# Kernel optimization log

Measured on AMD Instinct MI355X. Metric: run time of the kernel, lower is better.

Reference implementation:

```python
import jax, jax.numpy as jnp
import numpy as np

B, S, D = 32, 8192, 64


def setup_inputs() -> dict:
    key = jax.random.key(0)
    k1, k2 = jax.random.split(key)
    input_real = jax.random.normal(k1, (B, S, D), dtype=jnp.float32)
    input_imag = jax.random.normal(k2, (B, S, D), dtype=jnp.float32)
    return {"input_real": input_real, "input_imag": input_imag}


def reference(input_real, input_imag):
    # ComplexMixture: mean over seq of per-token complex outer products v v^H.
    # Original builds [B,S,D,D] via 4 batch_dots then means over S; fused here
    # as Gram contractions over the sequence axis (no [B,S,D,D] intermediate).
    seq_len = input_real.shape[1]
    inv_s = jnp.asarray(1.0 / seq_len, dtype=input_real.dtype)
    rr = jnp.einsum('bsi,bsj->bij', input_real, input_real)
    ii = jnp.einsum('bsi,bsj->bij', input_imag, input_imag)
    ri = jnp.einsum('bsi,bsj->bij', input_real, input_imag)
    out_real = (rr + ii) * inv_s                     # [B, D, D], symmetric
    out_imag = (ri - jnp.swapaxes(ri, 1, 2)) * inv_s  # [B, D, D], antisymmetric
    return (out_real, out_imag)
```

## Files before the change

kernel.cpp:

```cpp
#include <hip/hip_runtime.h>


#define BATCH  32
#define SEQ    8192
#define DD     64
#define CHUNKS 16
#define SCHUNK (SEQ / CHUNKS)
#define ROUNDS (SCHUNK / 64)

typedef __bf16 bf16x8 __attribute__((ext_vector_type(8)));
typedef float  f32x16 __attribute__((ext_vector_type(16)));

#define GLD_LDS16(gp, lp) \
  __builtin_amdgcn_global_load_lds( \
      (const __attribute__((address_space(1))) void*)(gp), \
      (__attribute__((address_space(3))) void*)(lp), 16, 0, 0)

__device__ __forceinline__ unsigned bf16pk(float a, float b) {
  unsigned ua = __builtin_bit_cast(unsigned, a);
  unsigned ub = __builtin_bit_cast(unsigned, b);
  ua = (ua + 0x7fffu + ((ua >> 16) & 1u)) >> 16;
  ub = (ub + 0x7fffu + ((ub >> 16) & 1u)) >> 16;
  return (ua & 0xffffu) | (ub << 16);
}

__device__ __forceinline__ bf16x8 ldsfrag(const float* p) {
  float f0 = p[0*64], f1 = p[1*64], f2 = p[2*64], f3 = p[3*64];
  float f4 = p[4*64], f5 = p[5*64], f6 = p[6*64], f7 = p[7*64];
  uint4 q;
  q.x = bf16pk(f0, f1); q.y = bf16pk(f2, f3);
  q.z = bf16pk(f4, f5); q.w = bf16pk(f6, f7);
  return __builtin_bit_cast(bf16x8, q);
}

#define MFMA(a, b, c) __builtin_amdgcn_mfma_f32_32x32x16_bf16((a), (b), (c), 0, 0, 0)

__global__ __launch_bounds__(256, 2) void gram_partial(
    const float* __restrict__ R, const float* __restrict__ I,
    float* __restrict__ ws)
{
  __shared__ float lds[16384];
  const int tid  = threadIdx.x;
  const int wave = tid >> 6;
  const int lane = tid & 63;
  const int l31  = lane & 31;
  const int lhi  = lane >> 5;
  const int b = blockIdx.x & 31;
  const int c = blockIdx.x >> 5;

  float* myb = lds + wave * 4096;
  const size_t g0 = (size_t)b * (SEQ * DD) + (size_t)(c * SCHUNK + wave * 16) * DD;
  const float* gR = R + g0;
  const float* gI = I + g0;

  f32x16 aS0 = {}, aS1 = {}, aS2 = {};
  f32x16 aM0 = {}, aM1 = {}, aM2 = {}, aM3 = {};

  auto ISSUE = [&](int rnd, int p) {
    const float* r = gR + (size_t)rnd * (64 * DD);
    const float* i = gI + (size_t)rnd * (64 * DD);
    float* d = myb + p * 2048;
    #pragma unroll
    for (int t = 0; t < 4; ++t) {
      GLD_LDS16(r + t * 256 + lane * 4, d + t * 256);
      GLD_LDS16(i + t * 256 + lane * 4, d + 1024 + t * 256);
    }
  };

  ISSUE(0, 0);
  #pragma unroll
  for (int r = 0; r < ROUNDS; ++r) {
    const int p = r & 1;
    if (r + 1 < ROUNDS) {
      ISSUE(r + 1, p ^ 1);
      asm volatile("s_waitcnt vmcnt(8)" ::: "memory");
    } else {
      asm volatile("s_waitcnt vmcnt(0)" ::: "memory");
    }
    const float* pR = myb + p * 2048 + (lhi * 8) * 64 + l31;
    const float* pI = pR + 1024;
    bf16x8 r0  = ldsfrag(pR),      r32 = ldsfrag(pR + 32);
    bf16x8 i0  = ldsfrag(pI),      i32 = ldsfrag(pI + 32);
    aS0 = MFMA(r0,  r0,  aS0);  aS0 = MFMA(i0,  i0,  aS0);
    aS1 = MFMA(r0,  r32, aS1);  aS1 = MFMA(i0,  i32, aS1);
    aS2 = MFMA(r32, r32, aS2);  aS2 = MFMA(i32, i32, aS2);
    aM0 = MFMA(r0,  i0,  aM0);
    aM1 = MFMA(r0,  i32, aM1);
    aM2 = MFMA(r32, i0,  aM2);
    aM3 = MFMA(r32, i32, aM3);
  }

  __syncthreads();
  float* Sp = lds;
  float* Mp = lds + 4160;
  for (int e = tid; e < 8320; e += 256) lds[e] = 0.0f;
  __syncthreads();
  #pragma unroll 1
  for (int w = 0; w < 4; ++w) {
    if (wave == w) {
      #pragma unroll
      for (int r = 0; r < 16; ++r) {
        const int ii = (r & 3) + 8 * (r >> 2) + 4 * lhi;
        const int jj = l31;
        Sp[ii * 65 + jj]              += aS0[r];
        Sp[ii * 65 + 32 + jj]         += aS1[r];
        Sp[(32 + ii) * 65 + 32 + jj]  += aS2[r];
        Mp[ii * 65 + jj]              += aM0[r];
        Mp[ii * 65 + 32 + jj]         += aM1[r];
        Mp[(32 + ii) * 65 + jj]       += aM2[r];
        Mp[(32 + ii) * 65 + 32 + jj]  += aM3[r];
      }
    }
    __syncthreads();
  }
  float* wsS = ws + ((size_t)(c * 32 + b) * 2) * 4096;
  float* wsM = wsS + 4096;
  #pragma unroll
  for (int k = 0; k < 16; ++k) {
    const int e = tid + 256 * k;
    const int i = e >> 6, j = e & 63;
    const float sv = (i >= 32 && j < 32) ? Sp[j * 65 + i] : Sp[i * 65 + j];
    wsS[e] = sv;
    wsM[e] = Mp[i * 65 + j] - Mp[j * 65 + i];
  }
}

__global__ __launch_bounds__(256) void gram_reduce(
    const float4* __restrict__ ws, float4* __restrict__ out)
{
  const int o = blockIdx.x * 256 + threadIdx.x;
  const int kind = o >> 15;
  const int rem  = o & 32767;
  const int b    = rem >> 10;
  const int e    = rem & 1023;
  const float inv = 1.0f / (float)SEQ;
  float sx = 0.f, sy = 0.f, sz = 0.f, sw = 0.f;
  #pragma unroll
  for (int c = 0; c < CHUNKS; ++c) {
    float4 v = ws[((size_t)(c * 32 + b) * 2 + kind) * 1024 + e];
    sx += v.x; sy += v.y; sz += v.z; sw += v.w;
  }
  float4 r; r.x = sx * inv; r.y = sy * inv; r.z = sz * inv; r.w = sw * inv;
  out[o] = r;
}

extern "C" void kernel_launch(void* const* d_in, const int* in_sizes, int n_in,
                              void* d_out, int out_size, void* d_ws, size_t ws_size,
                              hipStream_t stream) {
  const float* R = (const float*)d_in[0];
  const float* I = (const float*)d_in[1];
  float* out = (float*)d_out;
  float* ws  = (float*)d_ws;

  gram_partial<<<BATCH * CHUNKS, 256, 0, stream>>>(R, I, ws);
  gram_reduce<<<256, 256, 0, stream>>>((const float4*)ws, (float4*)out);
}
```

Before: 165.8 us.

## Drop LDS double buffering, raise occupancy, split sequence into more chunks

Removes the double-buffered global-to-LDS prefetch and halves shared memory per block. This lets launch bounds allow four blocks per CU, so latency is hidden by more resident waves instead of software pipelining. The sequence is split into 32 chunks when workspace allows, doubling the grid, and the reduce kernel now splits the chunk sum across four wave groups with an LDS combine. The cost is that each wave now stalls on its own loads every round, and the larger workspace means more partial-result traffic.

```diff
diff --git a/kernel.cpp b/kernel.cpp
--- a/kernel.cpp
+++ b/kernel.cpp
@@ -4,9 +4,6 @@
 #define BATCH  32
 #define SEQ    8192
 #define DD     64
-#define CHUNKS 16
-#define SCHUNK (SEQ / CHUNKS)
-#define ROUNDS (SCHUNK / 64)
 
 typedef __bf16 bf16x8 __attribute__((ext_vector_type(8)));
 typedef float  f32x16 __attribute__((ext_vector_type(16)));
@@ -35,11 +32,14 @@
 
 #define MFMA(a, b, c) __builtin_amdgcn_mfma_f32_32x32x16_bf16((a), (b), (c), 0, 0, 0)
 
-__global__ __launch_bounds__(256, 2) void gram_partial(
+template<int CHUNKS>
+__global__ __launch_bounds__(256, 4) void gram_partial(
     const float* __restrict__ R, const float* __restrict__ I,
     float* __restrict__ ws)
 {
-  __shared__ float lds[16384];
+  constexpr int SCHUNK = SEQ / CHUNKS;
+  constexpr int ROUNDS = SCHUNK / 64;
+  __shared__ float lds[8320];
   const int tid  = threadIdx.x;
   const int wave = tid >> 6;
   const int lane = tid & 63;
@@ -48,7 +48,7 @@
   const int b = blockIdx.x & 31;
   const int c = blockIdx.x >> 5;
 
-  float* myb = lds + wave * 4096;
+  float* myb = lds + wave * 2048;
   const size_t g0 = (size_t)b * (SEQ * DD) + (size_t)(c * SCHUNK + wave * 16) * DD;
   const float* gR = R + g0;
   const float* gI = I + g0;
@@ -56,31 +56,19 @@
   f32x16 aS0 = {}, aS1 = {}, aS2 = {};
   f32x16 aM0 = {}, aM1 = {}, aM2 = {}, aM3 = {};
 
-  auto ISSUE = [&](int rnd, int p) {
-    const float* r = gR + (size_t)rnd * (64 * DD);
-    const float* i = gI + (size_t)rnd * (64 * DD);
-    float* d = myb + p * 2048;
+  for (int r = 0; r < ROUNDS; ++r) {
+    const float* gr = gR + (size_t)r * (64 * DD);
+    const float* gi = gI + (size_t)r * (64 * DD);
     #pragma unroll
     for (int t = 0; t < 4; ++t) {
-      GLD_LDS16(r + t * 256 + lane * 4, d + t * 256);
-      GLD_LDS16(i + t * 256 + lane * 4, d + 1024 + t * 256);
+      GLD_LDS16(gr + t * 256 + lane * 4, myb + t * 256);
+      GLD_LDS16(gi + t * 256 + lane * 4, myb + 1024 + t * 256);
     }
-  };
-
-  ISSUE(0, 0);
-  #pragma unroll
-  for (int r = 0; r < ROUNDS; ++r) {
-    const int p = r & 1;
-    if (r + 1 < ROUNDS) {
-      ISSUE(r + 1, p ^ 1);
-      asm volatile("s_waitcnt vmcnt(8)" ::: "memory");
-    } else {
-      asm volatile("s_waitcnt vmcnt(0)" ::: "memory");
-    }
-    const float* pR = myb + p * 2048 + (lhi * 8) * 64 + l31;
+    asm volatile("s_waitcnt vmcnt(0)" ::: "memory");
+    const float* pR = myb + (lhi * 8) * 64 + l31;
     const float* pI = pR + 1024;
-    bf16x8 r0  = ldsfrag(pR),      r32 = ldsfrag(pR + 32);
-    bf16x8 i0  = ldsfrag(pI),      i32 = ldsfrag(pI + 32);
+    bf16x8 r0  = ldsfrag(pR),  r32 = ldsfrag(pR + 32);
+    bf16x8 i0  = ldsfrag(pI),  i32 = ldsfrag(pI + 32);
     aS0 = MFMA(r0,  r0,  aS0);  aS0 = MFMA(i0,  i0,  aS0);
     aS1 = MFMA(r0,  r32, aS1);  aS1 = MFMA(i0,  i32, aS1);
     aS2 = MFMA(r32, r32, aS2);  aS2 = MFMA(i32, i32, aS2);
@@ -88,6 +76,7 @@
     aM1 = MFMA(r0,  i32, aM1);
     aM2 = MFMA(r32, i0,  aM2);
     aM3 = MFMA(r32, i32, aM3);
+    asm volatile("s_waitcnt lgkmcnt(0)" ::: "memory");
   }
 
   __syncthreads();
@@ -125,23 +114,38 @@
   }
 }
 
+template<int CHUNKS>
 __global__ __launch_bounds__(256) void gram_reduce(
     const float4* __restrict__ ws, float4* __restrict__ out)
 {
-  const int o = blockIdx.x * 256 + threadIdx.x;
+  __shared__ float4 red[256];
+  const int t = threadIdx.x;
+  const int o = blockIdx.x * 64 + (t & 63);
+  const int q = t >> 6;
   const int kind = o >> 15;
   const int rem  = o & 32767;
   const int b    = rem >> 10;
   const int e    = rem & 1023;
-  const float inv = 1.0f / (float)SEQ;
   float sx = 0.f, sy = 0.f, sz = 0.f, sw = 0.f;
   #pragma unroll
-  for (int c = 0; c < CHUNKS; ++c) {
+  for (int cc = 0; cc < CHUNKS / 4; ++cc) {
+    const int c = q * (CHUNKS / 4) + cc;
     float4 v = ws[((size_t)(c * 32 + b) * 2 + kind) * 1024 + e];
     sx += v.x; sy += v.y; sz += v.z; sw += v.w;
   }
-  float4 r; r.x = sx * inv; r.y = sy * inv; r.z = sz * inv; r.w = sw * inv;
-  out[o] = r;
+  float4 p; p.x = sx; p.y = sy; p.z = sz; p.w = sw;
+  red[t] = p;
+  __syncthreads();
+  if (t < 64) {
+    const float inv = 1.0f / (float)SEQ;
+    float4 a = red[t], b2 = red[t + 64], c2 = red[t + 128], d = red[t + 192];
+    float4 r;
+    r.x = (a.x + b2.x + c2.x + d.x) * inv;
+    r.y = (a.y + b2.y + c2.y + d.y) * inv;
+    r.z = (a.z + b2.z + c2.z + d.z) * inv;
+    r.w = (a.w + b2.w + c2.w + d.w) * inv;
+    out[o] = r;
+  }
 }
 
 extern "C" void kernel_launch(void* const* d_in, const int* in_sizes, int n_in,
@@ -152,6 +156,12 @@
   float* out = (float*)d_out;
   float* ws  = (float*)d_ws;
 
-  gram_partial<<<BATCH * CHUNKS, 256, 0, stream>>>(R, I, ws);
-  gram_reduce<<<256, 256, 0, stream>>>((const float4*)ws, (float4*)out);
+  const size_t need32 = (size_t)32 * 32 * 2 * 4096 * 4;
+  if (ws_size >= need32) {
+    gram_partial<32><<<BATCH * 32, 256, 0, stream>>>(R, I, ws);
+    gram_reduce<32><<<1024, 256, 0, stream>>>((const float4*)ws, (float4*)out);
+  } else {
+    gram_partial<16><<<BATCH * 16, 256, 0, stream>>>(R, I, ws);
+    gram_reduce<16><<<512, 256, 0, stream>>>((const float4*)ws, (float4*)out);
+  }
 }
```

Result: slower. 241.0 us (+45.4%).
